# Optimization experiments

Hardware: AMD Instinct MI355X
Metric: run time of the kernel (lower is better)

## Reference

```python
import jax, jax.numpy as jnp
import numpy as np

N, E, IN, HID, HEADS, ED, OUT = 50000, 600000, 128, 64, 4, 16, 2
NEG_SLOPE = 0.2  # PyG GATv2Conv default negative_slope


def glorot(key, shape):
    fan_in, fan_out = shape[0], shape[-1]
    s = jnp.sqrt(6.0 / (fan_in + fan_out))
    return jax.random.uniform(key, shape, jnp.float32, -s, s)


def setup_inputs() -> dict:
    key = jax.random.key(0)
    ks = jax.random.split(key, 16)
    return {
        "x": jax.random.normal(ks[0], (N, IN), jnp.float32),
        "edge_index": jax.random.randint(ks[1], (2, E), 0, N, jnp.int32),
        "edge_attr": jax.random.normal(ks[2], (E, ED), jnp.float32),
        # conv1: GATv2Conv(IN -> HID, heads=HEADS, concat=True, edge_dim=ED)
        "W1l": glorot(ks[3], (IN, HEADS * HID)), "b1l": jnp.zeros((HEADS * HID,), jnp.float32),
        "W1r": glorot(ks[4], (IN, HEADS * HID)), "b1r": jnp.zeros((HEADS * HID,), jnp.float32),
        "W1e": glorot(ks[5], (ED, HEADS * HID)), "b1e": jnp.zeros((HEADS * HID,), jnp.float32),
        "att1": glorot(ks[6], (HEADS, HID)),
        "bias1": jnp.zeros((HEADS * HID,), jnp.float32),
        # conv2: GATv2Conv(HEADS*HID -> HID, heads=1, concat=False, edge_dim=ED)
        "W2l": glorot(ks[7], (HEADS * HID, HID)), "b2l": jnp.zeros((HID,), jnp.float32),
        "W2r": glorot(ks[8], (HEADS * HID, HID)), "b2r": jnp.zeros((HID,), jnp.float32),
        "W2e": glorot(ks[9], (ED, HID)), "b2e": jnp.zeros((HID,), jnp.float32),
        "att2": glorot(ks[10], (1, HID)),
        "bias2": jnp.zeros((HID,), jnp.float32),
        # edge MLP: Linear(2*HID+ED -> HID) -> ReLU -> Linear(HID -> OUT)
        "Wm1": glorot(ks[11], (2 * HID + ED, HID)), "bm1": jnp.zeros((HID,), jnp.float32),
        "Wm2": glorot(ks[12], (HID, OUT)), "bm2": jnp.zeros((OUT,), jnp.float32),
    }


def gatv2_layer(x, src, dst, edge_attr, Wl, bl, Wr, br, We, be, att, bias, heads, ch, concat):
    n = x.shape[0]
    xl = (x @ Wl + bl).reshape(n, heads, ch)          # lin_l(source)
    xr = (x @ Wr + br).reshape(n, heads, ch)          # lin_r(target)
    xe = (edge_attr @ We + be).reshape(-1, heads, ch)  # lin_edge(edge_attr)
    m = jax.nn.leaky_relu(xl[src] + xr[dst] + xe, NEG_SLOPE)   # [E, H, C]
    logits = jnp.einsum('ehc,hc->eh', m, att)                  # [E, H]
    # segment softmax over incoming edges of each target node
    amax = jax.lax.stop_gradient(jax.ops.segment_max(logits, dst, num_segments=n))
    ex = jnp.exp(logits - amax[dst])
    denom = jax.ops.segment_sum(ex, dst, num_segments=n)
    alpha = ex / denom[dst]                                    # [E, H]
    out = jax.ops.segment_sum(xl[src] * alpha[..., None], dst, num_segments=n)  # [N, H, C]
    out = out.reshape(n, heads * ch) if concat else out.mean(axis=1)
    return out + bias


def reference(x, edge_index, edge_attr, W1l, b1l, W1r, b1r, W1e, b1e, att1, bias1,
              W2l, b2l, W2r, b2r, W2e, b2e, att2, bias2, Wm1, bm1, Wm2, bm2):
    src, dst = edge_index[0], edge_index[1]
    h = jax.nn.relu(gatv2_layer(x, src, dst, edge_attr, W1l, b1l, W1r, b1r, W1e, b1e, att1, bias1, HEADS, HID, True))
    h = jax.nn.relu(gatv2_layer(h, src, dst, edge_attr, W2l, b2l, W2r, b2r, W2e, b2e, att2, bias2, 1, HID, False))
    ef = jnp.concatenate([h[src], h[dst], edge_attr], axis=1)  # [E, 2*HID+ED]
    return jax.nn.relu(ef @ Wm1 + bm1) @ Wm2 + bm2             # [E, OUT]
```

## Files before the change

kernel.cpp:

```cpp
#include <hip/hip_runtime.h>
#include <math.h>

#define NN 50000
#define EE 600000
#define IND 128
#define HIDD 64
#define NH 4
#define EDD 16
#define OUTD 2
#define C1 256

__device__ __forceinline__ float lrelu(float v){ return v > 0.f ? v : 0.2f*v; }
__device__ __forceinline__ unsigned short f2bf(float f){
    unsigned b = __float_as_uint(f);
    b += 0x7FFF + ((b >> 16) & 1);
    return (unsigned short)(b >> 16);
}
__device__ __forceinline__ float bf2f(unsigned short h){
    return __uint_as_float(((unsigned)h) << 16);
}

__global__ __launch_bounds__(256) void k_hist(const int* __restrict__ dst, int* __restrict__ cnt)
{
    int stride = gridDim.x * blockDim.x;
    for (int e = blockIdx.x * blockDim.x + threadIdx.x; e < EE; e += stride)
        atomicAdd(&cnt[dst[e]], 1);
}

__global__ __launch_bounds__(1024) void k_scan(const int* __restrict__ cnt, int* __restrict__ rs)
{
    __shared__ int wsum[16];
    __shared__ int wpref[16];
    int t = threadIdx.x, lane = t & 63, w = t >> 6;
    int running = 0;
    for (int base = 0; base < NN; base += 1024) {
        int idx = base + t;
        int v = (idx < NN) ? cnt[idx] : 0;
        int sc = v;
#pragma unroll
        for (int off = 1; off < 64; off <<= 1) {
            int u = __shfl_up(sc, off, 64);
            if (lane >= off) sc += u;
        }
        if (lane == 63) wsum[w] = sc;
        __syncthreads();
        if (w == 0 && lane < 16) {
            int x = wsum[lane];
#pragma unroll
            for (int off = 1; off < 16; off <<= 1) {
                int u = __shfl_up(x, off, 64);
                if (lane >= off) x += u;
            }
            wpref[lane] = x;
        }
        __syncthreads();
        int woff = (w == 0) ? 0 : wpref[w - 1];
        if (idx < NN) rs[idx] = running + woff + sc - v;
        running += wpref[15];
        __syncthreads();
    }
    if (t == 0) rs[NN] = running;
}

__global__ __launch_bounds__(256) void k_scatter(
    const int* __restrict__ src, const int* __restrict__ dst,
    const float* __restrict__ ea,
    const int* __restrict__ rs, int* __restrict__ cur,
    int* __restrict__ esrc, float* __restrict__ ea_s)
{
    int stride = gridDim.x * blockDim.x;
    for (int e = blockIdx.x * blockDim.x + threadIdx.x; e < EE; e += stride) {
        int d = dst[e];
        int p = rs[d] + atomicAdd(&cur[d], 1);
        esrc[p] = src[e];
        const float4* s4 = (const float4*)(ea + (size_t)e * EDD);
        float4* d4 = (float4*)(ea_s + (size_t)p * EDD);
        d4[0] = s4[0]; d4[1] = s4[1]; d4[2] = s4[2]; d4[3] = s4[3];
    }
}

__global__ __launch_bounds__(256) void k_lin1(
    const float* __restrict__ x, const float* __restrict__ Wl, const float* __restrict__ bl,
    const float* __restrict__ Wr, const float* __restrict__ br,
    unsigned short* __restrict__ xl, float* __restrict__ xr)
{
    __shared__ float As[16 * IND];
    int t = threadIdx.x;
    int row0 = blockIdx.x * 16;
#pragma unroll
    for (int j = 0; j < 8; ++j) {
        int idx = t + j * 256;
        int r = idx >> 7, c = idx & 127;
        As[idx] = (row0 + r < NN) ? x[(size_t)(row0 + r) * IND + c] : 0.f;
    }
    __syncthreads();
    float accl[16], accr[16];
    float bL = bl[t], bR = br[t];
#pragma unroll
    for (int i = 0; i < 16; ++i) { accl[i] = bL; accr[i] = bR; }
    for (int k = 0; k < IND; k += 4) {
        float wl0 = Wl[(k+0) * C1 + t], wl1 = Wl[(k+1) * C1 + t];
        float wl2 = Wl[(k+2) * C1 + t], wl3 = Wl[(k+3) * C1 + t];
        float wr0 = Wr[(k+0) * C1 + t], wr1 = Wr[(k+1) * C1 + t];
        float wr2 = Wr[(k+2) * C1 + t], wr3 = Wr[(k+3) * C1 + t];
#pragma unroll
        for (int i = 0; i < 16; ++i) {
            float4 a = *((const float4*)&As[i * IND + k]);
            accl[i] = fmaf(a.x, wl0, accl[i]); accl[i] = fmaf(a.y, wl1, accl[i]);
            accl[i] = fmaf(a.z, wl2, accl[i]); accl[i] = fmaf(a.w, wl3, accl[i]);
            accr[i] = fmaf(a.x, wr0, accr[i]); accr[i] = fmaf(a.y, wr1, accr[i]);
            accr[i] = fmaf(a.z, wr2, accr[i]); accr[i] = fmaf(a.w, wr3, accr[i]);
        }
    }
#pragma unroll
    for (int i = 0; i < 16; ++i) {
        int r = row0 + i;
        if (r < NN) {
            xl[(size_t)r * C1 + t] = f2bf(accl[i]);
            xr[(size_t)r * C1 + t] = accr[i];
        }
    }
}

#define GAT1_EDGE(XU, A0, A1, A2, A3) {                                        \
    float4 xl4 = make_float4(bf2f((XU).x), bf2f((XU).y), bf2f((XU).z), bf2f((XU).w)); \
    float ev[16] = {(A0).x,(A0).y,(A0).z,(A0).w,(A1).x,(A1).y,(A1).z,(A1).w,   \
                    (A2).x,(A2).y,(A2).z,(A2).w,(A3).x,(A3).y,(A3).z,(A3).w};  \
    float4 xe = sb4;                                                           \
    _Pragma("unroll")                                                          \
    for (int k = 0; k < 16; ++k) {                                             \
        xe.x = fmaf(ev[k], Wreg[k].x, xe.x);                                   \
        xe.y = fmaf(ev[k], Wreg[k].y, xe.y);                                   \
        xe.z = fmaf(ev[k], Wreg[k].z, xe.z);                                   \
        xe.w = fmaf(ev[k], Wreg[k].w, xe.w);                                   \
    }                                                                          \
    float vx = lrelu(xl4.x + xr4.x + xe.x);                                    \
    float vy = lrelu(xl4.y + xr4.y + xe.y);                                    \
    float vz = lrelu(xl4.z + xr4.z + xe.z);                                    \
    float vw = lrelu(xl4.w + xr4.w + xe.w);                                    \
    float p = vx * sa4.x + vy * sa4.y + vz * sa4.z + vw * sa4.w;               \
    p += __shfl_xor(p, 1, 64);                                                 \
    p += __shfl_xor(p, 2, 64);                                                 \
    p += __shfl_xor(p, 4, 64);                                                 \
    p += __shfl_xor(p, 8, 64);                                                 \
    float mn = fmaxf(m, p);                                                    \
    float scl = __expf(m - mn);                                                \
    float el  = __expf(p - mn);                                                \
    den = fmaf(den, scl, el);                                                  \
    acc.x = fmaf(acc.x, scl, el * xl4.x);                                      \
    acc.y = fmaf(acc.y, scl, el * xl4.y);                                      \
    acc.z = fmaf(acc.z, scl, el * xl4.z);                                      \
    acc.w = fmaf(acc.w, scl, el * xl4.w);                                      \
    m = mn;                                                                    \
}

__global__ __launch_bounds__(256, 3) void k_gat1(
    const int* __restrict__ rs, const int* __restrict__ esrc,
    const float* __restrict__ ea_s, const float* __restrict__ We, const float* __restrict__ be,
    const float* __restrict__ att, const unsigned short* __restrict__ xl,
    const float* __restrict__ xr, float* __restrict__ h1)
{
    int t = threadIdx.x, lane = t & 63, w = t >> 6;
    int c4 = lane * 4;
    float4 Wreg[16];
#pragma unroll
    for (int k = 0; k < 16; ++k) Wreg[k] = *((const float4*)(We + k * C1 + c4));
    float4 sb4 = *((const float4*)(be + c4));
    float4 sa4 = *((const float4*)(att + c4));
    for (int n = blockIdx.x * 4 + w; n < NN; n += gridDim.x * 4) {
        int beg = __builtin_amdgcn_readfirstlane(rs[n]);
        int end = __builtin_amdgcn_readfirstlane(rs[n + 1]);
        float4 xr4 = *((const float4*)(xr + (size_t)n * C1 + c4));
        float m = -INFINITY, den = 0.f;
        float4 acc = make_float4(0.f, 0.f, 0.f, 0.f);
        int i = beg;
        for (; i + 2 <= end; i += 2) {
            int s0 = esrc[i], s1 = esrc[i + 1];
            ushort4 xu0 = *((const ushort4*)(xl + (size_t)s0 * C1 + c4));
            ushort4 xu1 = *((const ushort4*)(xl + (size_t)s1 * C1 + c4));
            const float* ep = ea_s + (size_t)i * EDD;
            float4 a00 = *((const float4*)(ep +  0));
            float4 a01 = *((const float4*)(ep +  4));
            float4 a02 = *((const float4*)(ep +  8));
            float4 a03 = *((const float4*)(ep + 12));
            float4 a10 = *((const float4*)(ep + 16));
            float4 a11 = *((const float4*)(ep + 20));
            float4 a12 = *((const float4*)(ep + 24));
            float4 a13 = *((const float4*)(ep + 28));
            GAT1_EDGE(xu0, a00, a01, a02, a03);
            GAT1_EDGE(xu1, a10, a11, a12, a13);
        }
        if (i < end) {
            int s0 = esrc[i];
            ushort4 xu0 = *((const ushort4*)(xl + (size_t)s0 * C1 + c4));
            const float* ep = ea_s + (size_t)i * EDD;
            float4 a00 = *((const float4*)(ep +  0));
            float4 a01 = *((const float4*)(ep +  4));
            float4 a02 = *((const float4*)(ep +  8));
            float4 a03 = *((const float4*)(ep + 12));
            GAT1_EDGE(xu0, a00, a01, a02, a03);
        }
        float r = den > 0.f ? 1.f / den : 0.f;
        float4 o = make_float4(acc.x * r, acc.y * r, acc.z * r, acc.w * r);
        *((float4*)(h1 + (size_t)n * C1 + c4)) = o;
    }
}

__global__ __launch_bounds__(256) void k_lin2(
    const float* __restrict__ h1acc, const float* __restrict__ bias1,
    const float* __restrict__ Wl, const float* __restrict__ bl,
    const float* __restrict__ Wr, const float* __restrict__ br,
    unsigned short* __restrict__ xl2, float* __restrict__ xr2)
{
    __shared__ float As[16 * 260];
    int t = threadIdx.x;
    int row0 = blockIdx.x * 16;
    float b1 = bias1[t];
#pragma unroll
    for (int j = 0; j < 16; ++j) {
        float v = (row0 + j < NN) ? h1acc[(size_t)(row0 + j) * C1 + t] : 0.f;
        v = v + b1;
        As[j * 260 + t] = v > 0.f ? v : 0.f;
    }
    __syncthreads();
    int col = t & 63, g = t >> 6;
    float accl[4], accr[4];
    float bL = bl[col], bR = br[col];
#pragma unroll
    for (int i = 0; i < 4; ++i) { accl[i] = bL; accr[i] = bR; }
    for (int k = 0; k < C1; k += 4) {
        float wl0 = Wl[(k+0) * HIDD + col], wl1 = Wl[(k+1) * HIDD + col];
        float wl2 = Wl[(k+2) * HIDD + col], wl3 = Wl[(k+3) * HIDD + col];
        float wr0 = Wr[(k+0) * HIDD + col], wr1 = Wr[(k+1) * HIDD + col];
        float wr2 = Wr[(k+2) * HIDD + col], wr3 = Wr[(k+3) * HIDD + col];
#pragma unroll
        for (int i = 0; i < 4; ++i) {
            float4 a = *((const float4*)&As[(g * 4 + i) * 260 + k]);
            accl[i] = fmaf(a.x, wl0, accl[i]); accl[i] = fmaf(a.y, wl1, accl[i]);
            accl[i] = fmaf(a.z, wl2, accl[i]); accl[i] = fmaf(a.w, wl3, accl[i]);
            accr[i] = fmaf(a.x, wr0, accr[i]); accr[i] = fmaf(a.y, wr1, accr[i]);
            accr[i] = fmaf(a.z, wr2, accr[i]); accr[i] = fmaf(a.w, wr3, accr[i]);
        }
    }
#pragma unroll
    for (int i = 0; i < 4; ++i) {
        int r = row0 + g * 4 + i;
        if (r < NN) {
            xl2[(size_t)r * HIDD + col] = f2bf(accl[i]);
            xr2[(size_t)r * HIDD + col] = accr[i];
        }
    }
}

#define GAT2_EDGE(XU, A0, A1, A2, A3) {                                        \
    float xlv = bf2f(XU);                                                      \
    float ev[16] = {(A0).x,(A0).y,(A0).z,(A0).w,(A1).x,(A1).y,(A1).z,(A1).w,   \
                    (A2).x,(A2).y,(A2).z,(A2).w,(A3).x,(A3).y,(A3).z,(A3).w};  \
    float xe = bev;                                                            \
    _Pragma("unroll")                                                          \
    for (int k = 0; k < 16; ++k) xe = fmaf(ev[k], Wreg[k], xe);                \
    float v = lrelu(xlv + xrv + xe);                                           \
    float p = v * sav;                                                         \
    p += __shfl_xor(p, 1, 64);                                                 \
    p += __shfl_xor(p, 2, 64);                                                 \
    p += __shfl_xor(p, 4, 64);                                                 \
    p += __shfl_xor(p, 8, 64);                                                 \
    p += __shfl_xor(p, 16, 64);                                                \
    p += __shfl_xor(p, 32, 64);                                                \
    float mn = fmaxf(m, p);                                                    \
    float scl = __expf(m - mn);                                                \
    float el  = __expf(p - mn);                                                \
    den = fmaf(den, scl, el);                                                  \
    acc = fmaf(acc, scl, el * xlv);                                            \
    m = mn;                                                                    \
}

__global__ __launch_bounds__(256) void k_gat2(
    const int* __restrict__ rs, const int* __restrict__ esrc,
    const float* __restrict__ ea_s, const float* __restrict__ We, const float* __restrict__ be,
    const float* __restrict__ att, const unsigned short* __restrict__ xl,
    const float* __restrict__ xr, const float* __restrict__ bias2, float* __restrict__ h2)
{
    int t = threadIdx.x, lane = t & 63, w = t >> 6;
    float Wreg[16];
#pragma unroll
    for (int k = 0; k < 16; ++k) Wreg[k] = We[k * HIDD + lane];
    float bev = be[lane], sav = att[lane], b2 = bias2[lane];
    for (int n = blockIdx.x * 4 + w; n < NN; n += gridDim.x * 4) {
        int beg = __builtin_amdgcn_readfirstlane(rs[n]);
        int end = __builtin_amdgcn_readfirstlane(rs[n + 1]);
        float xrv = xr[(size_t)n * HIDD + lane];
        float m = -INFINITY, den = 0.f, acc = 0.f;
        int i = beg;
        for (; i + 2 <= end; i += 2) {
            int s0 = esrc[i], s1 = esrc[i + 1];
            unsigned short xu0 = xl[(size_t)s0 * HIDD + lane];
            unsigned short xu1 = xl[(size_t)s1 * HIDD + lane];
            const float* ep = ea_s + (size_t)i * EDD;
            float4 a00 = *((const float4*)(ep +  0));
            float4 a01 = *((const float4*)(ep +  4));
            float4 a02 = *((const float4*)(ep +  8));
            float4 a03 = *((const float4*)(ep + 12));
            float4 a10 = *((const float4*)(ep + 16));
            float4 a11 = *((const float4*)(ep + 20));
            float4 a12 = *((const float4*)(ep + 24));
            float4 a13 = *((const float4*)(ep + 28));
            GAT2_EDGE(xu0, a00, a01, a02, a03);
            GAT2_EDGE(xu1, a10, a11, a12, a13);
        }
        if (i < end) {
            int s0 = esrc[i];
            unsigned short xu0 = xl[(size_t)s0 * HIDD + lane];
            const float* ep = ea_s + (size_t)i * EDD;
            float4 a00 = *((const float4*)(ep +  0));
            float4 a01 = *((const float4*)(ep +  4));
            float4 a02 = *((const float4*)(ep +  8));
            float4 a03 = *((const float4*)(ep + 12));
            GAT2_EDGE(xu0, a00, a01, a02, a03);
        }
        float r = den > 0.f ? 1.f / den : 0.f;
        float o = fmaf(acc, r, b2);
        h2[(size_t)n * HIDD + lane] = o > 0.f ? o : 0.f;
    }
}

__global__ __launch_bounds__(256) void k_pq(
    const float* __restrict__ h2, const float* __restrict__ Wm1,
    unsigned short* __restrict__ P, unsigned short* __restrict__ Q)
{
    __shared__ float As[16 * 68];
    int t = threadIdx.x;
    int row0 = blockIdx.x * 16;
    {
        int r = t >> 4, cc = (t & 15) * 4;
        float4 v = *((const float4*)(h2 + (size_t)(row0 + r) * HIDD + cc));
        *((float4*)&As[r * 68 + cc]) = v;
    }
    __syncthreads();
    int col = t & 63, g = t >> 6;
    float accP[4] = {0.f, 0.f, 0.f, 0.f}, accQ[4] = {0.f, 0.f, 0.f, 0.f};
    for (int k = 0; k < 64; k += 4) {
        float wp0 = Wm1[(k+0) * HIDD + col], wp1 = Wm1[(k+1) * HIDD + col];
        float wp2 = Wm1[(k+2) * HIDD + col], wp3 = Wm1[(k+3) * HIDD + col];
        float wq0 = Wm1[(64+k+0) * HIDD + col], wq1 = Wm1[(64+k+1) * HIDD + col];
        float wq2 = Wm1[(64+k+2) * HIDD + col], wq3 = Wm1[(64+k+3) * HIDD + col];
#pragma unroll
        for (int i = 0; i < 4; ++i) {
            float4 a = *((const float4*)&As[(g * 4 + i) * 68 + k]);
            accP[i] = fmaf(a.x, wp0, accP[i]); accP[i] = fmaf(a.y, wp1, accP[i]);
            accP[i] = fmaf(a.z, wp2, accP[i]); accP[i] = fmaf(a.w, wp3, accP[i]);
            accQ[i] = fmaf(a.x, wq0, accQ[i]); accQ[i] = fmaf(a.y, wq1, accQ[i]);
            accQ[i] = fmaf(a.z, wq2, accQ[i]); accQ[i] = fmaf(a.w, wq3, accQ[i]);
        }
    }
#pragma unroll
    for (int i = 0; i < 4; ++i) {
        int r = row0 + g * 4 + i;
        P[(size_t)r * HIDD + col] = f2bf(accP[i]);
        Q[(size_t)r * HIDD + col] = f2bf(accQ[i]);
    }
}

__global__ __launch_bounds__(256, 3) void k_edge(
    const int* __restrict__ src, const int* __restrict__ dst,
    const unsigned short* __restrict__ P, const unsigned short* __restrict__ Q,
    const float* __restrict__ ea,
    const float* __restrict__ Wm1, const float* __restrict__ bm1,
    const float* __restrict__ Wm2, const float* __restrict__ bm2,
    float* __restrict__ out)
{
    int t = threadIdx.x, lane = t & 63, w = t >> 6;
    int sub = lane & 15, grp = lane >> 4;
    int c4 = sub * 4;
    float4 Wreg[16];
#pragma unroll
    for (int k = 0; k < 16; ++k) Wreg[k] = *((const float4*)(Wm1 + (size_t)(128 + k) * HIDD + c4));
    float4 b1 = *((const float4*)(bm1 + c4));
    float w200 = Wm2[(c4+0)*2], w201 = Wm2[(c4+0)*2+1];
    float w210 = Wm2[(c4+1)*2], w211 = Wm2[(c4+1)*2+1];
    float w220 = Wm2[(c4+2)*2], w221 = Wm2[(c4+2)*2+1];
    float w230 = Wm2[(c4+3)*2], w231 = Wm2[(c4+3)*2+1];
    float b20 = bm2[0], b21 = bm2[1];
    for (int base = blockIdx.x * 16 + w * 4; base < EE; base += gridDim.x * 16) {
        int e = base + grp;
        int s = src[e], d = dst[e];
        ushort4 pu = *((const ushort4*)(P + (size_t)s * HIDD + c4));
        ushort4 qu = *((const ushort4*)(Q + (size_t)d * HIDD + c4));
        float4 ea0 = *((const float4*)(ea + (size_t)e * EDD));
        float4 ea1 = *((const float4*)(ea + (size_t)e * EDD + 4));
        float4 ea2 = *((const float4*)(ea + (size_t)e * EDD + 8));
        float4 ea3 = *((const float4*)(ea + (size_t)e * EDD + 12));
        float ev[16] = {ea0.x, ea0.y, ea0.z, ea0.w, ea1.x, ea1.y, ea1.z, ea1.w,
                        ea2.x, ea2.y, ea2.z, ea2.w, ea3.x, ea3.y, ea3.z, ea3.w};
        float4 hsum = b1;
#pragma unroll
        for (int k = 0; k < 16; ++k) {
            hsum.x = fmaf(ev[k], Wreg[k].x, hsum.x);
            hsum.y = fmaf(ev[k], Wreg[k].y, hsum.y);
            hsum.z = fmaf(ev[k], Wreg[k].z, hsum.z);
            hsum.w = fmaf(ev[k], Wreg[k].w, hsum.w);
        }
        float hx = fmaxf(hsum.x + bf2f(pu.x) + bf2f(qu.x), 0.f);
        float hy = fmaxf(hsum.y + bf2f(pu.y) + bf2f(qu.y), 0.f);
        float hz = fmaxf(hsum.z + bf2f(pu.z) + bf2f(qu.z), 0.f);
        float hw = fmaxf(hsum.w + bf2f(pu.w) + bf2f(qu.w), 0.f);
        float p0 = hx * w200 + hy * w210 + hz * w220 + hw * w230;
        float p1 = hx * w201 + hy * w211 + hz * w221 + hw * w231;
        p0 += __shfl_xor(p0, 1, 64);
        p0 += __shfl_xor(p0, 2, 64);
        p0 += __shfl_xor(p0, 4, 64);
        p0 += __shfl_xor(p0, 8, 64);
        p1 += __shfl_xor(p1, 1, 64);
        p1 += __shfl_xor(p1, 2, 64);
        p1 += __shfl_xor(p1, 4, 64);
        p1 += __shfl_xor(p1, 8, 64);
        if (sub == 0) ((float2*)out)[e] = make_float2(p0 + b20, p1 + b21);
    }
}

extern "C" void kernel_launch(void* const* d_in, const int* in_sizes, int n_in,
                              void* d_out, int out_size, void* d_ws, size_t ws_size,
                              hipStream_t stream)
{
    const float* x    = (const float*)d_in[0];
    const int*   ei   = (const int*)d_in[1];
    const float* ea   = (const float*)d_in[2];
    const float* W1l  = (const float*)d_in[3];
    const float* b1l  = (const float*)d_in[4];
    const float* W1r  = (const float*)d_in[5];
    const float* b1r  = (const float*)d_in[6];
    const float* W1e  = (const float*)d_in[7];
    const float* b1e  = (const float*)d_in[8];
    const float* att1 = (const float*)d_in[9];
    const float* bias1= (const float*)d_in[10];
    const float* W2l  = (const float*)d_in[11];
    const float* b2l  = (const float*)d_in[12];
    const float* W2r  = (const float*)d_in[13];
    const float* b2r  = (const float*)d_in[14];
    const float* W2e  = (const float*)d_in[15];
    const float* b2e  = (const float*)d_in[16];
    const float* att2 = (const float*)d_in[17];
    const float* bias2= (const float*)d_in[18];
    const float* Wm1  = (const float*)d_in[19];
    const float* bm1  = (const float*)d_in[20];
    const float* Wm2  = (const float*)d_in[21];
    const float* bm2  = (const float*)d_in[22];
    float* out = (float*)d_out;
    const int* srcp = ei;
    const int* dstp = ei + EE;

    float* ws = (float*)d_ws;
    const size_t NC1  = (size_t)NN * C1;
    const size_t NH64 = (size_t)NN * HIDD;
    size_t o_xl1u = 0;
    size_t o_xr1  = o_xl1u + NC1 / 2;
    size_t o_xl2u = 0;
    size_t o_xr2  = o_xl2u + NH64 / 2;
    size_t o_h2   = o_xr2 + NH64;
    size_t o_Pu   = o_h2 + NH64;
    size_t o_Qu   = o_Pu + NH64 / 2;
    size_t o_h1   = o_xr1 + NC1;
    size_t o_ea_s = o_h1 + NC1;
    size_t o_cnt  = o_ea_s + (size_t)EE * EDD;
    size_t o_rs   = o_cnt + 2 * (size_t)NN;
    size_t o_esrc = o_rs + (size_t)NN + 8;

    unsigned short* xl1u = (unsigned short*)(ws + o_xl1u);
    unsigned short* xl2u = (unsigned short*)(ws + o_xl2u);
    unsigned short* Pu   = (unsigned short*)(ws + o_Pu);
    unsigned short* Qu   = (unsigned short*)(ws + o_Qu);
    float* ea_s = ws + o_ea_s;
    int* cnt  = (int*)(ws + o_cnt);
    int* cur  = cnt + NN;
    int* rs   = (int*)(ws + o_rs);
    int* esrc = (int*)(ws + o_esrc);

    hipMemsetAsync(cnt, 0, 2 * (size_t)NN * sizeof(int), stream);

    dim3 blk(256);
    k_hist<<<1024, blk, 0, stream>>>(dstp, cnt);
    k_scan<<<1, 1024, 0, stream>>>(cnt, rs);
    k_scatter<<<1024, blk, 0, stream>>>(srcp, dstp, ea, rs, cur, esrc, ea_s);

    k_lin1<<<3125, blk, 0, stream>>>(x, W1l, b1l, W1r, b1r, xl1u, ws + o_xr1);
    k_gat1<<<2048, blk, 0, stream>>>(rs, esrc, ea_s, W1e, b1e, att1,
                                     xl1u, ws + o_xr1, ws + o_h1);
    k_lin2<<<3125, blk, 0, stream>>>(ws + o_h1, bias1, W2l, b2l, W2r, b2r,
                                     xl2u, ws + o_xr2);
    k_gat2<<<2048, blk, 0, stream>>>(rs, esrc, ea_s, W2e, b2e, att2,
                                     xl2u, ws + o_xr2, bias2, ws + o_h2);
    k_pq<<<3125, blk, 0, stream>>>(ws + o_h2, Wm1, Pu, Qu);
    k_edge<<<2048, blk, 0, stream>>>(srcp, dstp, Pu, Qu, ea,
                                     Wm1, bm1, Wm2, bm2, out);
}
```

Measured before the change: 663.6 us.

## Store edge attributes as fp16 and use packed fdot2 for edge projections

The scatter kernel now converts edge attributes to fp16 in two copies, one CSR-sorted and one in original order. The gat1, gat2 and edge-MLP kernels read these half-size buffers and compute the 16-wide edge projection with v_dot2 fp16 instructions against fp16-converted weights. This halves edge-attribute traffic and halves the FMA count per edge in the three edge-heavy kernels. The cost is reduced precision in the edge projection and an extra fp16 copy written during scatter.

```diff
diff --git a/kernel.cpp b/kernel.cpp
--- a/kernel.cpp
+++ b/kernel.cpp
@@ -10,6 +10,8 @@
 #define OUTD 2
 #define C1 256
 
+typedef _Float16 h2 __attribute__((ext_vector_type(2)));
+
 __device__ __forceinline__ float lrelu(float v){ return v > 0.f ? v : 0.2f*v; }
 __device__ __forceinline__ unsigned short f2bf(float f){
     unsigned b = __float_as_uint(f);
@@ -18,6 +20,19 @@
 }
 __device__ __forceinline__ float bf2f(unsigned short h){
     return __uint_as_float(((unsigned)h) << 16);
+}
+
+#if defined(__has_builtin)
+#if __has_builtin(__builtin_amdgcn_fdot2)
+#define HAS_FDOT2 1
+#endif
+#endif
+__device__ __forceinline__ float fdot2(h2 a, h2 b, float c){
+#ifdef HAS_FDOT2
+    return __builtin_amdgcn_fdot2(a, b, c, false);
+#else
+    return fmaf((float)a[1], (float)b[1], fmaf((float)a[0], (float)b[0], c));
+#endif
 }
 
 __global__ __launch_bounds__(256) void k_hist(const int* __restrict__ dst, int* __restrict__ cnt)
@@ -66,7 +81,7 @@
     const int* __restrict__ src, const int* __restrict__ dst,
     const float* __restrict__ ea,
     const int* __restrict__ rs, int* __restrict__ cur,
-    int* __restrict__ esrc, float* __restrict__ ea_s)
+    int* __restrict__ esrc, _Float16* __restrict__ ea_s, _Float16* __restrict__ ea_h)
 {
     int stride = gridDim.x * blockDim.x;
     for (int e = blockIdx.x * blockDim.x + threadIdx.x; e < EE; e += stride) {
@@ -74,8 +89,20 @@
         int p = rs[d] + atomicAdd(&cur[d], 1);
         esrc[p] = src[e];
         const float4* s4 = (const float4*)(ea + (size_t)e * EDD);
-        float4* d4 = (float4*)(ea_s + (size_t)p * EDD);
-        d4[0] = s4[0]; d4[1] = s4[1]; d4[2] = s4[2]; d4[3] = s4[3];
+        float4 a0 = s4[0], a1 = s4[1], a2 = s4[2], a3 = s4[3];
+        union { h2 h[8]; uint4 u[2]; } pk;
+        pk.h[0][0] = (_Float16)a0.x; pk.h[0][1] = (_Float16)a0.y;
+        pk.h[1][0] = (_Float16)a0.z; pk.h[1][1] = (_Float16)a0.w;
+        pk.h[2][0] = (_Float16)a1.x; pk.h[2][1] = (_Float16)a1.y;
+        pk.h[3][0] = (_Float16)a1.z; pk.h[3][1] = (_Float16)a1.w;
+        pk.h[4][0] = (_Float16)a2.x; pk.h[4][1] = (_Float16)a2.y;
+        pk.h[5][0] = (_Float16)a2.z; pk.h[5][1] = (_Float16)a2.w;
+        pk.h[6][0] = (_Float16)a3.x; pk.h[6][1] = (_Float16)a3.y;
+        pk.h[7][0] = (_Float16)a3.z; pk.h[7][1] = (_Float16)a3.w;
+        uint4* dq = (uint4*)(ea_s + (size_t)p * EDD);
+        dq[0] = pk.u[0]; dq[1] = pk.u[1];
+        uint4* hq = (uint4*)(ea_h + (size_t)e * EDD);
+        hq[0] = pk.u[0]; hq[1] = pk.u[1];
     }
 }
 
@@ -122,22 +149,22 @@
     }
 }
 
-#define GAT1_EDGE(XU, A0, A1, A2, A3) {                                        \
+#define GAT1_EDGE(XU, U0, U1) {                                                \
     float4 xl4 = make_float4(bf2f((XU).x), bf2f((XU).y), bf2f((XU).z), bf2f((XU).w)); \
-    float ev[16] = {(A0).x,(A0).y,(A0).z,(A0).w,(A1).x,(A1).y,(A1).z,(A1).w,   \
-                    (A2).x,(A2).y,(A2).z,(A2).w,(A3).x,(A3).y,(A3).z,(A3).w};  \
-    float4 xe = sb4;                                                           \
+    union { uint4 u[2]; h2 h[8]; } eu_; eu_.u[0] = (U0); eu_.u[1] = (U1);      \
+    float xex = sb4.x, xey = sb4.y, xez = sb4.z, xew = sb4.w;                  \
     _Pragma("unroll")                                                          \
-    for (int k = 0; k < 16; ++k) {                                             \
-        xe.x = fmaf(ev[k], Wreg[k].x, xe.x);                                   \
-        xe.y = fmaf(ev[k], Wreg[k].y, xe.y);                                   \
-        xe.z = fmaf(ev[k], Wreg[k].z, xe.z);                                   \
-        xe.w = fmaf(ev[k], Wreg[k].w, xe.w);                                   \
+    for (int kk = 0; kk < 8; ++kk) {                                           \
+        h2 ev2 = eu_.h[kk];                                                    \
+        xex = fdot2(ev2, Wh[0][kk], xex);                                      \
+        xey = fdot2(ev2, Wh[1][kk], xey);                                      \
+        xez = fdot2(ev2, Wh[2][kk], xez);                                      \
+        xew = fdot2(ev2, Wh[3][kk], xew);                                      \
     }                                                                          \
-    float vx = lrelu(xl4.x + xr4.x + xe.x);                                    \
-    float vy = lrelu(xl4.y + xr4.y + xe.y);                                    \
-    float vz = lrelu(xl4.z + xr4.z + xe.z);                                    \
-    float vw = lrelu(xl4.w + xr4.w + xe.w);                                    \
+    float vx = lrelu(xl4.x + xr4.x + xex);                                     \
+    float vy = lrelu(xl4.y + xr4.y + xey);                                     \
+    float vz = lrelu(xl4.z + xr4.z + xez);                                     \
+    float vw = lrelu(xl4.w + xr4.w + xew);                                     \
     float p = vx * sa4.x + vy * sa4.y + vz * sa4.z + vw * sa4.w;               \
     p += __shfl_xor(p, 1, 64);                                                 \
     p += __shfl_xor(p, 2, 64);                                                 \
@@ -156,15 +183,21 @@
 
 __global__ __launch_bounds__(256, 3) void k_gat1(
     const int* __restrict__ rs, const int* __restrict__ esrc,
-    const float* __restrict__ ea_s, const float* __restrict__ We, const float* __restrict__ be,
+    const _Float16* __restrict__ ea_s, const float* __restrict__ We, const float* __restrict__ be,
     const float* __restrict__ att, const unsigned short* __restrict__ xl,
     const float* __restrict__ xr, float* __restrict__ h1)
 {
     int t = threadIdx.x, lane = t & 63, w = t >> 6;
     int c4 = lane * 4;
-    float4 Wreg[16];
-#pragma unroll
-    for (int k = 0; k < 16; ++k) Wreg[k] = *((const float4*)(We + k * C1 + c4));
+    h2 Wh[4][8];
+#pragma unroll
+    for (int k = 0; k < 16; ++k) {
+        float4 wv = *((const float4*)(We + k * C1 + c4));
+        Wh[0][k>>1][k&1] = (_Float16)wv.x;
+        Wh[1][k>>1][k&1] = (_Float16)wv.y;
+        Wh[2][k>>1][k&1] = (_Float16)wv.z;
+        Wh[3][k>>1][k&1] = (_Float16)wv.w;
+    }
     float4 sb4 = *((const float4*)(be + c4));
     float4 sa4 = *((const float4*)(att + c4));
     for (int n = blockIdx.x * 4 + w; n < NN; n += gridDim.x * 4) {
@@ -178,27 +211,18 @@
             int s0 = esrc[i], s1 = esrc[i + 1];
             ushort4 xu0 = *((const ushort4*)(xl + (size_t)s0 * C1 + c4));
             ushort4 xu1 = *((const ushort4*)(xl + (size_t)s1 * C1 + c4));
-            const float* ep = ea_s + (size_t)i * EDD;
-            float4 a00 = *((const float4*)(ep +  0));
-            float4 a01 = *((const float4*)(ep +  4));
-            float4 a02 = *((const float4*)(ep +  8));
-            float4 a03 = *((const float4*)(ep + 12));
-            float4 a10 = *((const float4*)(ep + 16));
-            float4 a11 = *((const float4*)(ep + 20));
-            float4 a12 = *((const float4*)(ep + 24));
-            float4 a13 = *((const float4*)(ep + 28));
-            GAT1_EDGE(xu0, a00, a01, a02, a03);
-            GAT1_EDGE(xu1, a10, a11, a12, a13);
+            const uint4* ep = (const uint4*)(ea_s + (size_t)i * EDD);
+            uint4 u00 = ep[0], u01 = ep[1];
+            uint4 u10 = ep[2], u11 = ep[3];
+            GAT1_EDGE(xu0, u00, u01);
+            GAT1_EDGE(xu1, u10, u11);
         }
         if (i < end) {
             int s0 = esrc[i];
             ushort4 xu0 = *((const ushort4*)(xl + (size_t)s0 * C1 + c4));
-            const float* ep = ea_s + (size_t)i * EDD;
-            float4 a00 = *((const float4*)(ep +  0));
-            float4 a01 = *((const float4*)(ep +  4));
-            float4 a02 = *((const float4*)(ep +  8));
-            float4 a03 = *((const float4*)(ep + 12));
-            GAT1_EDGE(xu0, a00, a01, a02, a03);
+            const uint4* ep = (const uint4*)(ea_s + (size_t)i * EDD);
+            uint4 u00 = ep[0], u01 = ep[1];
+            GAT1_EDGE(xu0, u00, u01);
         }
         float r = den > 0.f ? 1.f / den : 0.f;
         float4 o = make_float4(acc.x * r, acc.y * r, acc.z * r, acc.w * r);
@@ -252,13 +276,12 @@
     }
 }
 
-#define GAT2_EDGE(XU, A0, A1, A2, A3) {                                        \
+#define GAT2_EDGE(XU, U0, U1) {                                                \
     float xlv = bf2f(XU);                                                      \
-    float ev[16] = {(A0).x,(A0).y,(A0).z,(A0).w,(A1).x,(A1).y,(A1).z,(A1).w,   \
-                    (A2).x,(A2).y,(A2).z,(A2).w,(A3).x,(A3).y,(A3).z,(A3).w};  \
+    union { uint4 u[2]; h2 h[8]; } eu_; eu_.u[0] = (U0); eu_.u[1] = (U1);      \
     float xe = bev;                                                            \
     _Pragma("unroll")                                                          \
-    for (int k = 0; k < 16; ++k) xe = fmaf(ev[k], Wreg[k], xe);                \
+    for (int kk = 0; kk < 8; ++kk) xe = fdot2(eu_.h[kk], Wh2[kk], xe);         \
     float v = lrelu(xlv + xrv + xe);                                           \
     float p = v * sav;                                                         \
     p += __shfl_xor(p, 1, 64);                                                 \
@@ -277,14 +300,14 @@
 
 __global__ __launch_bounds__(256) void k_gat2(
     const int* __restrict__ rs, const int* __restrict__ esrc,
-    const float* __restrict__ ea_s, const float* __restrict__ We, const float* __restrict__ be,
+    const _Float16* __restrict__ ea_s, const float* __restrict__ We, const float* __restrict__ be,
     const float* __restrict__ att, const unsigned short* __restrict__ xl,
-    const float* __restrict__ xr, const float* __restrict__ bias2, float* __restrict__ h2)
+    const float* __restrict__ xr, const float* __restrict__ bias2, float* __restrict__ h2v)
 {
     int t = threadIdx.x, lane = t & 63, w = t >> 6;
-    float Wreg[16];
-#pragma unroll
-    for (int k = 0; k < 16; ++k) Wreg[k] = We[k * HIDD + lane];
+    h2 Wh2[8];
+#pragma unroll
+    for (int k = 0; k < 16; ++k) Wh2[k>>1][k&1] = (_Float16)We[k * HIDD + lane];
     float bev = be[lane], sav = att[lane], b2 = bias2[lane];
     for (int n = blockIdx.x * 4 + w; n < NN; n += gridDim.x * 4) {
         int beg = __builtin_amdgcn_readfirstlane(rs[n]);
@@ -296,31 +319,22 @@
             int s0 = esrc[i], s1 = esrc[i + 1];
             unsigned short xu0 = xl[(size_t)s0 * HIDD + lane];
             unsigned short xu1 = xl[(size_t)s1 * HIDD + lane];
-            const float* ep = ea_s + (size_t)i * EDD;
-            float4 a00 = *((const float4*)(ep +  0));
-            float4 a01 = *((const float4*)(ep +  4));
-            float4 a02 = *((const float4*)(ep +  8));
-            float4 a03 = *((const float4*)(ep + 12));
-            float4 a10 = *((const float4*)(ep + 16));
-            float4 a11 = *((const float4*)(ep + 20));
-            float4 a12 = *((const float4*)(ep + 24));
-            float4 a13 = *((const float4*)(ep + 28));
-            GAT2_EDGE(xu0, a00, a01, a02, a03);
-            GAT2_EDGE(xu1, a10, a11, a12, a13);
+            const uint4* ep = (const uint4*)(ea_s + (size_t)i * EDD);
+            uint4 u00 = ep[0], u01 = ep[1];
+            uint4 u10 = ep[2], u11 = ep[3];
+            GAT2_EDGE(xu0, u00, u01);
+            GAT2_EDGE(xu1, u10, u11);
         }
         if (i < end) {
             int s0 = esrc[i];
             unsigned short xu0 = xl[(size_t)s0 * HIDD + lane];
-            const float* ep = ea_s + (size_t)i * EDD;
-            float4 a00 = *((const float4*)(ep +  0));
-            float4 a01 = *((const float4*)(ep +  4));
-            float4 a02 = *((const float4*)(ep +  8));
-            float4 a03 = *((const float4*)(ep + 12));
-            GAT2_EDGE(xu0, a00, a01, a02, a03);
+            const uint4* ep = (const uint4*)(ea_s + (size_t)i * EDD);
+            uint4 u00 = ep[0], u01 = ep[1];
+            GAT2_EDGE(xu0, u00, u01);
         }
         float r = den > 0.f ? 1.f / den : 0.f;
         float o = fmaf(acc, r, b2);
-        h2[(size_t)n * HIDD + lane] = o > 0.f ? o : 0.f;
+        h2v[(size_t)n * HIDD + lane] = o > 0.f ? o : 0.f;
     }
 }
 
@@ -364,7 +378,7 @@
 __global__ __launch_bounds__(256, 3) void k_edge(
     const int* __restrict__ src, const int* __restrict__ dst,
     const unsigned short* __restrict__ P, const unsigned short* __restrict__ Q,
-    const float* __restrict__ ea,
+    const _Float16* __restrict__ ea_h,
     const float* __restrict__ Wm1, const float* __restrict__ bm1,
     const float* __restrict__ Wm2, const float* __restrict__ bm2,
     float* __restrict__ out)
@@ -372,9 +386,15 @@
     int t = threadIdx.x, lane = t & 63, w = t >> 6;
     int sub = lane & 15, grp = lane >> 4;
     int c4 = sub * 4;
-    float4 Wreg[16];
-#pragma unroll
-    for (int k = 0; k < 16; ++k) Wreg[k] = *((const float4*)(Wm1 + (size_t)(128 + k) * HIDD + c4));
+    h2 Wh[4][8];
+#pragma unroll
+    for (int k = 0; k < 16; ++k) {
+        float4 wv = *((const float4*)(Wm1 + (size_t)(128 + k) * HIDD + c4));
+        Wh[0][k>>1][k&1] = (_Float16)wv.x;
+        Wh[1][k>>1][k&1] = (_Float16)wv.y;
+        Wh[2][k>>1][k&1] = (_Float16)wv.z;
+        Wh[3][k>>1][k&1] = (_Float16)wv.w;
+    }
     float4 b1 = *((const float4*)(bm1 + c4));
     float w200 = Wm2[(c4+0)*2], w201 = Wm2[(c4+0)*2+1];
     float w210 = Wm2[(c4+1)*2], w211 = Wm2[(c4+1)*2+1];
@@ -386,19 +406,17 @@
         int s = src[e], d = dst[e];
         ushort4 pu = *((const ushort4*)(P + (size_t)s * HIDD + c4));
         ushort4 qu = *((const ushort4*)(Q + (size_t)d * HIDD + c4));
-        float4 ea0 = *((const float4*)(ea + (size_t)e * EDD));
-        float4 ea1 = *((const float4*)(ea + (size_t)e * EDD + 4));
-        float4 ea2 = *((const float4*)(ea + (size_t)e * EDD + 8));
-        float4 ea3 = *((const float4*)(ea + (size_t)e * EDD + 12));
-        float ev[16] = {ea0.x, ea0.y, ea0.z, ea0.w, ea1.x, ea1.y, ea1.z, ea1.w,
-                        ea2.x, ea2.y, ea2.z, ea2.w, ea3.x, ea3.y, ea3.z, ea3.w};
+        union { uint4 u[2]; h2 h[8]; } eu_;
+        const uint4* ep = (const uint4*)(ea_h + (size_t)e * EDD);
+        eu_.u[0] = ep[0]; eu_.u[1] = ep[1];
         float4 hsum = b1;
 #pragma unroll
-        for (int k = 0; k < 16; ++k) {
-            hsum.x = fmaf(ev[k], Wreg[k].x, hsum.x);
-            hsum.y = fmaf(ev[k], Wreg[k].y, hsum.y);
-            hsum.z = fmaf(ev[k], Wreg[k].z, hsum.z);
-            hsum.w = fmaf(ev[k], Wreg[k].w, hsum.w);
+        for (int kk = 0; kk < 8; ++kk) {
+            h2 ev2 = eu_.h[kk];
+            hsum.x = fdot2(ev2, Wh[0][kk], hsum.x);
+            hsum.y = fdot2(ev2, Wh[1][kk], hsum.y);
+            hsum.z = fdot2(ev2, Wh[2][kk], hsum.z);
+            hsum.w = fdot2(ev2, Wh[3][kk], hsum.w);
         }
         float hx = fmaxf(hsum.x + bf2f(pu.x) + bf2f(qu.x), 0.f);
         float hy = fmaxf(hsum.y + bf2f(pu.y) + bf2f(qu.y), 0.f);
@@ -452,6 +470,7 @@
     float* ws = (float*)d_ws;
     const size_t NC1  = (size_t)NN * C1;
     const size_t NH64 = (size_t)NN * HIDD;
+    const size_t EAH  = (size_t)EE * EDD / 2;
     size_t o_xl1u = 0;
     size_t o_xr1  = o_xl1u + NC1 / 2;
     size_t o_xl2u = 0;
@@ -461,7 +480,8 @@
     size_t o_Qu   = o_Pu + NH64 / 2;
     size_t o_h1   = o_xr1 + NC1;
     size_t o_ea_s = o_h1 + NC1;
-    size_t o_cnt  = o_ea_s + (size_t)EE * EDD;
+    size_t o_ea_h = o_ea_s + EAH;
+    size_t o_cnt  = o_ea_h + EAH;
     size_t o_rs   = o_cnt + 2 * (size_t)NN;
     size_t o_esrc = o_rs + (size_t)NN + 8;
 
@@ -469,7 +489,8 @@
     unsigned short* xl2u = (unsigned short*)(ws + o_xl2u);
     unsigned short* Pu   = (unsigned short*)(ws + o_Pu);
     unsigned short* Qu   = (unsigned short*)(ws + o_Qu);
-    float* ea_s = ws + o_ea_s;
+    _Float16* ea_s = (_Float16*)(ws + o_ea_s);
+    _Float16* ea_h = (_Float16*)(ws + o_ea_h);
     int* cnt  = (int*)(ws + o_cnt);
     int* cur  = cnt + NN;
     int* rs   = (int*)(ws + o_rs);
@@ -480,7 +501,7 @@
     dim3 blk(256);
     k_hist<<<1024, blk, 0, stream>>>(dstp, cnt);
     k_scan<<<1, 1024, 0, stream>>>(cnt, rs);
-    k_scatter<<<1024, blk, 0, stream>>>(srcp, dstp, ea, rs, cur, esrc, ea_s);
+    k_scatter<<<1024, blk, 0, stream>>>(srcp, dstp, ea, rs, cur, esrc, ea_s, ea_h);
 
     k_lin1<<<3125, blk, 0, stream>>>(x, W1l, b1l, W1r, b1r, xl1u, ws + o_xr1);
     k_gat1<<<2048, blk, 0, stream>>>(rs, esrc, ea_s, W1e, b1e, att1,
@@ -490,6 +511,6 @@
     k_gat2<<<2048, blk, 0, stream>>>(rs, esrc, ea_s, W2e, b2e, att2,
                                      xl2u, ws + o_xr2, bias2, ws + o_h2);
     k_pq<<<3125, blk, 0, stream>>>(ws + o_h2, Wm1, Pu, Qu);
-    k_edge<<<2048, blk, 0, stream>>>(srcp, dstp, Pu, Qu, ea,
+    k_edge<<<2048, blk, 0, stream>>>(srcp, dstp, Pu, Qu, ea_h,
                                      Wm1, bm1, Wm2, bm2, out);
 }
```

Result: no change. 663.4 us (-0.0%).
